# Performance work log

Hardware: AMD Instinct MI355X
Metric: run time of the kernel (lower is better)

Reference implementation:

```python
import jax, jax.numpy as jnp
import numpy as np
import math

B, S, D_IN, D_ATTN, D_HID = 4, 2048, 1024, 1024, 1024

def gelu_erf(x):
    return 0.5 * x * (1.0 + jax.lax.erf(x / math.sqrt(2.0)))

def setup_inputs() -> dict:
    key = jax.random.key(0)
    k = jax.random.split(key, 8)
    inputs = jax.random.normal(k[0], (B, S, D_IN), dtype=jnp.float32)
    attn_mask = jax.random.randint(k[1], (B, S, S), 0, 2, dtype=jnp.int32)
    sq = 1.0 / math.sqrt(D_IN)
    Wq = jax.random.normal(k[2], (D_IN, D_ATTN), dtype=jnp.float32) * sq
    bq = jnp.zeros((D_ATTN,), dtype=jnp.float32)
    Wk = jax.random.normal(k[3], (D_IN, D_ATTN), dtype=jnp.float32) * sq
    bk = jnp.zeros((D_ATTN,), dtype=jnp.float32)
    Wv = jax.random.normal(k[4], (D_IN, D_HID), dtype=jnp.float32) * sq
    bv = jnp.zeros((D_HID,), dtype=jnp.float32)
    return {"inputs": inputs, "attn_mask": attn_mask,
            "Wq": Wq, "bq": bq, "Wk": Wk, "bk": bk, "Wv": Wv, "bv": bv}

def reference(inputs, attn_mask, Wq, bq, Wk, bk, Wv, bv):
    # Q, K: [B, S, d_k]
    Q = inputs @ Wq + bq
    K = inputs @ Wk + bk
    scores = jnp.einsum('bqd,bkd->bqk', Q, K) / math.sqrt(D_ATTN)
    scores = scores + attn_mask.astype(scores.dtype) * (-1e9)
    attn = jax.nn.softmax(scores, axis=-1)
    WV = gelu_erf(inputs @ Wv + bv)           # [B, S, hidden]
    context = jnp.einsum('bqk,bkh->bqh', attn, WV)
    return (context, attn)
```

## Files before the change

kernel.cpp:

```cpp
#include <hip/hip_runtime.h>
#include <hip/hip_bf16.h>
#include <math.h>

#define B_   4
#define S_   2048
#define DIN  1024
#define DATT 1024
#define DHID 1024

typedef short bf16x8 __attribute__((ext_vector_type(8)));
typedef float f32x4  __attribute__((ext_vector_type(4)));

__device__ inline unsigned short f2bf(float f) {
    unsigned u = __float_as_uint(f);
    u += 0x7fffu + ((u >> 16) & 1u);
    return (unsigned short)(u >> 16);
}
__device__ inline float bf2f(unsigned u16) {
    return __uint_as_float(u16 << 16);
}
__device__ inline void gld16(const void* g, void* l) {
    __builtin_amdgcn_global_load_lds(
        (const __attribute__((address_space(1))) unsigned int*)g,
        (__attribute__((address_space(3))) unsigned int*)l, 16, 0, 0);
}

__device__ inline void xmap(int& bx, int& by, int& z)
{
    int gx = gridDim.x, gy = gridDim.y;
    int nwg = gx * gy * gridDim.z;
    int lin = blockIdx.x + gx * (blockIdx.y + gy * blockIdx.z);
    int s = (nwg & 7) ? lin : ((lin & 7) * (nwg >> 3) + (lin >> 3));
    if (!(gx & 3) && !(gy & 1)) {
        int cpz = (gx >> 2) * (gy >> 1);
        int chunk = s >> 3, w = s & 7;
        int cz = chunk / cpz, c2 = chunk % cpz;
        int cx = c2 % (gx >> 2), cy = c2 / (gx >> 2);
        bx = cx * 4 + (w & 3);
        by = cy * 2 + (w >> 2);
        z  = cz;
    } else {
        bx = s % gx;
        int t = s / gx;
        by = t % gy;
        z  = t / gy;
    }
}

__global__ __launch_bounds__(256)
void prep_k(const float* __restrict__ x, unsigned short* __restrict__ xb,
            const float* __restrict__ Wq, const float* __restrict__ Wk,
            const float* __restrict__ Wv, unsigned short* __restrict__ Wt,
            const int* __restrict__ m, unsigned* __restrict__ mb)
{
    const int b = blockIdx.x;
    const int tid = threadIdx.x;
    if (b < 4096) {
        int i = b * 256 + tid;
        const float4* p = (const float4*)x + (size_t)i * 2;
        float4 v0 = p[0], v1 = p[1];
        uint4 o;
        o.x = (unsigned)f2bf(v0.x) | ((unsigned)f2bf(v0.y) << 16);
        o.y = (unsigned)f2bf(v0.z) | ((unsigned)f2bf(v0.w) << 16);
        o.z = (unsigned)f2bf(v1.x) | ((unsigned)f2bf(v1.y) << 16);
        o.w = (unsigned)f2bf(v1.z) | ((unsigned)f2bf(v1.w) << 16);
        ((uint4*)xb)[i] = o;
    } else if (b < 4864) {
        int idx = b - 4096;
        int w = idx >> 8;
        const float* W = (w == 0) ? Wq : ((w == 1) ? Wk : Wv);
        unsigned short* D = Wt + (size_t)w * DIN * DATT;
        int t = (idx & 255) * 256 + tid;
        int n  = t >> 6;
        int kc = (t & 63) * 16;
        unsigned short r[16];
#pragma unroll
        for (int i = 0; i < 16; ++i) r[i] = f2bf(W[(size_t)(kc + i) * DATT + n]);
        uint4 o0, o1;
        o0.x = (unsigned)r[0] | ((unsigned)r[1] << 16);  o0.y = (unsigned)r[2] | ((unsigned)r[3] << 16);
        o0.z = (unsigned)r[4] | ((unsigned)r[5] << 16);  o0.w = (unsigned)r[6] | ((unsigned)r[7] << 16);
        o1.x = (unsigned)r[8] | ((unsigned)r[9] << 16);  o1.y = (unsigned)r[10] | ((unsigned)r[11] << 16);
        o1.z = (unsigned)r[12] | ((unsigned)r[13] << 16); o1.w = (unsigned)r[14] | ((unsigned)r[15] << 16);
        *(uint4*)(D + (size_t)n * DIN + kc)     = o0;
        *(uint4*)(D + (size_t)n * DIN + kc + 8) = o1;
    } else {
        int w = (b - 4864) * 256 + tid;
        const uint4* p = (const uint4*)(m + (size_t)w * 32);
        unsigned bits = 0;
#pragma unroll
        for (int g = 0; g < 8; ++g) {
            uint4 v = p[g];
            bits |= (v.x ? 1u : 0u) << (g * 4 + 0);
            bits |= (v.y ? 1u : 0u) << (g * 4 + 1);
            bits |= (v.z ? 1u : 0u) << (g * 4 + 2);
            bits |= (v.w ? 1u : 0u) << (g * 4 + 3);
        }
        mb[w] = bits;
    }
}

template<int EPI>
__global__ __launch_bounds__(512, 4)
void gemmS_k(const unsigned short* __restrict__ Ap, const unsigned short* __restrict__ Bp,
             const float* __restrict__ b0, const float* __restrict__ b1,
             const float* __restrict__ b2, const unsigned* __restrict__ mbits,
             void* __restrict__ Cp, void* __restrict__ Cp2,
             int K, int lda, int ldb, int ldc,
             long aStride, long bStride, long cStride, float scale)
{
    __shared__ __align__(16) unsigned short Al[256][64];
    __shared__ __align__(16) unsigned short Bl[128][64];

    int bx, by, z;
    xmap(bx, by, z);
    const int tid  = threadIdx.x;
    const int row0 = by * 256;
    const int col0 = bx * 128;
    const int wid  = tid >> 6, lane = tid & 63;
    const int lr = lane & 15, lg = lane >> 4;
    const int wm = wid >> 1, wn = wid & 1;
    const int wb = (tid & 448) * 16;

    const unsigned short* Ab = Ap + (size_t)aStride * z;
    const unsigned short* Bb = Bp + (size_t)bStride * z;

    f32x4 acc[4][4] = {};
    const int nt = K >> 6;

    const int srow = tid >> 3, sj = tid & 7;

    for (int t = 0; t < nt; ++t) {
        const int k0 = t << 6;
#pragma unroll
        for (int r = 0; r < 4; ++r) {
            int row = r * 64 + srow;
            gld16(Ab + (size_t)(row0 + row) * lda + k0 + ((sj ^ (row & 7)) << 3),
                  (char*)&Al[0][0] + r * 8192 + wb);
        }
#pragma unroll
        for (int r = 0; r < 2; ++r) {
            int row = r * 64 + srow;
            gld16(Bb + (size_t)(col0 + row) * ldb + k0 + ((sj ^ (row & 7)) << 3),
                  (char*)&Bl[0][0] + r * 8192 + wb);
        }
        __syncthreads();
#pragma unroll
        for (int s = 0; s < 2; ++s) {
            bf16x8 av[4], bv[4];
#pragma unroll
            for (int i = 0; i < 4; ++i) {
                int ra = wm * 64 + i * 16 + lr;
                av[i] = *(const bf16x8*)((const char*)&Al[0][0] + ra * 128 + ((((s << 2) | lg) ^ (ra & 7)) << 4));
                int rb = wn * 64 + i * 16 + lr;
                bv[i] = *(const bf16x8*)((const char*)&Bl[0][0] + rb * 128 + ((((s << 2) | lg) ^ (rb & 7)) << 4));
            }
#pragma unroll
            for (int mi = 0; mi < 4; ++mi)
#pragma unroll
                for (int ni = 0; ni < 4; ++ni)
                    acc[mi][ni] = __builtin_amdgcn_mfma_f32_16x16x32_bf16(av[mi], bv[ni], acc[mi][ni], 0, 0, 0);
        }
        __syncthreads();
    }

    unsigned short* scr = &Al[0][0] + wid * 2048;

    if (EPI == 6) {
        int w = col0 >> 10;
        if (w < 2) {
            unsigned short* C = (unsigned short*)Cp + (size_t)w * ((size_t)B_ * S_ * DATT);
            const float* bias = w ? b1 : b0;
            int cb0 = (col0 & 1023) + wn * 64;
#pragma unroll
            for (int h = 0; h < 2; ++h) {
#pragma unroll
                for (int mm = 0; mm < 2; ++mm) {
                    int mi = h * 2 + mm;
#pragma unroll
                    for (int ni = 0; ni < 4; ++ni) {
                        int lcol = ni * 16 + lr;
                        float bb = bias[cb0 + lcol];
#pragma unroll
                        for (int v = 0; v < 4; ++v) {
                            int wrow = mm * 16 + lg * 4 + v;
                            scr[wrow * 64 + (((lcol >> 3) ^ (wrow & 7)) << 3) + (lcol & 7)] =
                                f2bf(acc[mi][ni][v] + bb);
                        }
                    }
                }
                asm volatile("s_waitcnt lgkmcnt(0)" ::: "memory");
#pragma unroll
                for (int rr = 0; rr < 4; ++rr) {
                    int lrow = rr * 8 + (lane >> 3);
                    int chunk = lane & 7;
                    uint4 u = *(const uint4*)&scr[lrow * 64 + ((chunk ^ (lrow & 7)) << 3)];
                    int grow = row0 + wm * 64 + h * 32 + lrow;
                    *(uint4*)(C + (size_t)grow * DATT + cb0 + chunk * 8) = u;
                }
                asm volatile("s_waitcnt lgkmcnt(0)" ::: "memory");
            }
        } else {
            unsigned short* C = (unsigned short*)Cp2;
            int zz = row0 >> 11;
            int sb0 = (row0 & 2047) + wm * 64;
            int hb0 = (col0 & 1023) + wn * 64;
#pragma unroll
            for (int h = 0; h < 2; ++h) {
#pragma unroll
                for (int nn = 0; nn < 2; ++nn) {
                    int ni = h * 2 + nn;
                    int lcol = nn * 16 + lr;
                    float bb = b2[hb0 + h * 32 + lcol];
#pragma unroll
                    for (int mi = 0; mi < 4; ++mi)
#pragma unroll
                        for (int v = 0; v < 4; ++v) {
                            int lrow = mi * 16 + lg * 4 + v;
                            float xv = acc[mi][ni][v] + bb;
                            xv = 0.5f * xv * (1.0f + erff(xv * 0.70710678118654752f));
                            scr[lcol * 64 + (((lrow >> 3) ^ (lcol & 7)) << 3) + (lrow & 7)] = f2bf(xv);
                        }
                }
                asm volatile("s_waitcnt lgkmcnt(0)" ::: "memory");
#pragma unroll
                for (int rr = 0; rr < 4; ++rr) {
                    int lhid = rr * 8 + (lane >> 3);
                    int chunk = lane & 7;
                    uint4 u = *(const uint4*)&scr[lhid * 64 + ((chunk ^ (lhid & 7)) << 3)];
                    int ghid = hb0 + h * 32 + lhid;
                    *(uint4*)(C + ((size_t)zz * DHID + ghid) * S_ + sb0 + chunk * 8) = u;
                }
                asm volatile("s_waitcnt lgkmcnt(0)" ::: "memory");
            }
        }
    } else {
        unsigned short* C = (unsigned short*)Cp + (size_t)cStride * z;
        const unsigned* mb = mbits + (size_t)z * (S_ * S_ / 32);
        const int wbase = (col0 + wn * 64) >> 5;
#pragma unroll
        for (int h = 0; h < 2; ++h) {
#pragma unroll
            for (int mm = 0; mm < 2; ++mm) {
                int mi = h * 2 + mm;
#pragma unroll
                for (int v = 0; v < 4; ++v) {
                    int row = row0 + wm * 64 + mi * 16 + lg * 4 + v;
                    unsigned w0 = mb[(size_t)row * (S_ / 32) + wbase];
                    unsigned w1 = mb[(size_t)row * (S_ / 32) + wbase + 1];
                    int wrow = mm * 16 + lg * 4 + v;
#pragma unroll
                    for (int ni = 0; ni < 4; ++ni) {
                        int lcol = ni * 16 + lr;
                        unsigned wsel = (ni & 2) ? w1 : w0;
                        float ev = ((wsel >> ((ni & 1) * 16 + lr)) & 1)
                                 ? 0.0f : __expf(acc[mi][ni][v] * scale);
                        scr[wrow * 64 + (((lcol >> 3) ^ (wrow & 7)) << 3) + (lcol & 7)] = f2bf(ev);
                    }
                }
            }
            asm volatile("s_waitcnt lgkmcnt(0)" ::: "memory");
#pragma unroll
            for (int rr = 0; rr < 4; ++rr) {
                int lrow = rr * 8 + (lane >> 3);
                int chunk = lane & 7;
                uint4 u = *(const uint4*)&scr[lrow * 64 + ((chunk ^ (lrow & 7)) << 3)];
                int grow = row0 + wm * 64 + h * 32 + lrow;
                *(uint4*)(C + (size_t)grow * ldc + col0 + wn * 64 + chunk * 8) = u;
            }
            asm volatile("s_waitcnt lgkmcnt(0)" ::: "memory");
        }
    }
}

template<int AMODE, int EPI>
__global__ __launch_bounds__(256)
void gemm_k(const void* __restrict__ Ap, const unsigned short* __restrict__ Bp,
            const float* __restrict__ b0, const float* __restrict__ b1,
            const float* __restrict__ b2, const int* __restrict__ maskp,
            void* __restrict__ Cp, void* __restrict__ Cp2,
            int K, int lda, int ldb, int ldc,
            long aStride, long bStride, long cStride, long mStride, float scale)
{
    __shared__ __align__(16) unsigned short sh[2][2][128][64];
    int bx, by, z;
    xmap(bx, by, z);
    const int tid  = threadIdx.x;
    const int row0 = by * 128;
    const int col0 = bx * 128;
    const int wave = tid >> 6, lane = tid & 63;
    const int lr = lane & 15, lg = lane >> 4;
    const int wm = (wave >> 1) * 64, wn = (wave & 1) * 64;
    const unsigned short* Bb = Bp + (size_t)bStride * z;
    f32x4 acc[4][4] = {};
    const int nt = K >> 6;
    auto stage = [&](int b, int k0) {
        if (AMODE == 0) {
            const unsigned short* A = (const unsigned short*)Ap + (size_t)aStride * z;
#pragma unroll
            for (int q = 0; q < 4; ++q) {
                int c = q * 256 + tid;
                int row = c >> 3, j = c & 7;
                gld16((const char*)(A + (size_t)(row0 + row) * lda + k0) + ((j ^ (row & 7)) << 4),
                      (char*)&sh[b][0][0][0] + ((q * 256 + (tid & 192)) << 4));
            }
        } else {
            const float* A = (const float*)Ap + (size_t)aStride * z;
#pragma unroll
            for (int q = 0; q < 4; ++q) {
                int c = q * 256 + tid;
                int row = c >> 3, j = c & 7;
                const float* src = A + (size_t)(row0 + row) * lda + k0 + ((j ^ (row & 7)) << 3);
                float4 v0 = *(const float4*)src;
                float4 v1 = *(const float4*)(src + 4);
                uint4 p;
                p.x = (unsigned)f2bf(v0.x) | ((unsigned)f2bf(v0.y) << 16);
                p.y = (unsigned)f2bf(v0.z) | ((unsigned)f2bf(v0.w) << 16);
                p.z = (unsigned)f2bf(v1.x) | ((unsigned)f2bf(v1.y) << 16);
                p.w = (unsigned)f2bf(v1.z) | ((unsigned)f2bf(v1.w) << 16);
                *(uint4*)((char*)&sh[b][0][0][0] + ((size_t)c << 4)) = p;
            }
        }
#pragma unroll
        for (int q = 0; q < 4; ++q) {
            int c = q * 256 + tid;
            int row = c >> 3, j = c & 7;
            gld16((const char*)(Bb + (size_t)(col0 + row) * ldb + k0) + ((j ^ (row & 7)) << 4),
                  (char*)&sh[b][1][0][0] + ((q * 256 + (tid & 192)) << 4));
        }
    };
    stage(0, 0);
    __syncthreads();
    int cur = 0;
    for (int t = 0; t < nt; ++t) {
        if (t + 1 < nt) stage(cur ^ 1, (t + 1) << 6);
        const char* baseA = (const char*)&sh[cur][0][0][0];
        const char* baseB = (const char*)&sh[cur][1][0][0];
        bf16x8 af[2][4], bfv[2][4];
#pragma unroll
        for (int s = 0; s < 2; ++s)
#pragma unroll
            for (int i = 0; i < 4; ++i) {
                int ra = wm + i * 16 + lr;
                af[s][i]  = *(const bf16x8*)(baseA + ra * 128 + ((((s << 2) | lg) ^ (ra & 7)) << 4));
                int rb = wn + i * 16 + lr;
                bfv[s][i] = *(const bf16x8*)(baseB + rb * 128 + ((((s << 2) | lg) ^ (rb & 7)) << 4));
            }
#pragma unroll
        for (int s = 0; s < 2; ++s)
#pragma unroll
            for (int mi = 0; mi < 4; ++mi)
#pragma unroll
                for (int ni = 0; ni < 4; ++ni)
                    acc[mi][ni] = __builtin_amdgcn_mfma_f32_16x16x32_bf16(af[s][mi], bfv[s][ni], acc[mi][ni], 0, 0, 0);
        if (t + 1 < nt) __syncthreads();
        cur ^= 1;
    }
    if (EPI == 6) {
        int w = col0 >> 10;
        int cb = (col0 & 1023) + wn;
        if (w < 2) {
            unsigned short* C = (unsigned short*)Cp + (size_t)w * ((size_t)B_ * S_ * DATT);
            const float* bias = w ? b1 : b0;
#pragma unroll
            for (int mi = 0; mi < 4; ++mi)
#pragma unroll
                for (int ni = 0; ni < 4; ++ni) {
                    int col = cb + ni * 16 + lr;
                    float bb = bias[col];
                    int rowb = row0 + wm + mi * 16 + lg * 4;
#pragma unroll
                    for (int v = 0; v < 4; ++v)
                        C[(size_t)(rowb + v) * DATT + col] = f2bf(acc[mi][ni][v] + bb);
                }
        } else {
            unsigned short* C = (unsigned short*)Cp2;
            int zz = row0 >> 11;
            int sb = (row0 & 2047) + wm;
#pragma unroll
            for (int mi = 0; mi < 4; ++mi)
#pragma unroll
                for (int ni = 0; ni < 4; ++ni) {
                    int col = cb + ni * 16 + lr;
                    float bb = b2[col];
                    unsigned short r[4];
#pragma unroll
                    for (int v = 0; v < 4; ++v) {
                        float xv = acc[mi][ni][v] + bb;
                        xv = 0.5f * xv * (1.0f + erff(xv * 0.70710678118654752f));
                        r[v] = f2bf(xv);
                    }
                    uint2 o;
                    o.x = (unsigned)r[0] | ((unsigned)r[1] << 16);
                    o.y = (unsigned)r[2] | ((unsigned)r[3] << 16);
                    *(uint2*)(C + ((size_t)zz * DHID + col) * S_ + sb + mi * 16 + lg * 4) = o;
                }
        }
    } else if (EPI == 5) {
        float* C = (float*)Cp + (size_t)cStride * z;
        const float* invs = b0 + (size_t)z * S_;
#pragma unroll
        for (int mi = 0; mi < 4; ++mi)
#pragma unroll
            for (int ni = 0; ni < 4; ++ni) {
                int col = col0 + wn + ni * 16 + lr;
                int rowb = row0 + wm + mi * 16 + lg * 4;
#pragma unroll
                for (int v = 0; v < 4; ++v)
                    C[(size_t)(rowb + v) * ldc + col] = acc[mi][ni][v] * invs[rowb + v];
            }
    } else {
        float* C = (float*)Cp + (size_t)cStride * z;
        const int* mp = (EPI == 2) ? (maskp + (size_t)mStride * z) : nullptr;
#pragma unroll
        for (int mi = 0; mi < 4; ++mi)
#pragma unroll
            for (int ni = 0; ni < 4; ++ni) {
                int col = col0 + wn + ni * 16 + lr;
                int rowb = row0 + wm + mi * 16 + lg * 4;
#pragma unroll
                for (int v = 0; v < 4; ++v) {
                    float val = acc[mi][ni][v];
                    if (EPI == 2) val = val * scale + (float)mp[(size_t)(rowb + v) * ldc + col] * (-1e9f);
                    C[(size_t)(rowb + v) * ldc + col] = val;
                }
            }
    }
}

__global__ __launch_bounds__(256)
void rownormM_k(const unsigned short* __restrict__ e, float* __restrict__ attn,
                float* __restrict__ invs)
{
    const int row = blockIdx.x;
    const int tid = threadIdx.x;
    uint4 u = ((const uint4*)(e + (size_t)row * S_))[tid];
    float f[8];
    f[0] = bf2f(u.x & 0xffffu); f[1] = bf2f(u.x >> 16);
    f[2] = bf2f(u.y & 0xffffu); f[3] = bf2f(u.y >> 16);
    f[4] = bf2f(u.z & 0xffffu); f[5] = bf2f(u.z >> 16);
    f[6] = bf2f(u.w & 0xffffu); f[7] = bf2f(u.w >> 16);
    float s = ((f[0] + f[1]) + (f[2] + f[3])) + ((f[4] + f[5]) + (f[6] + f[7]));
#pragma unroll
    for (int o = 32; o; o >>= 1) s += __shfl_xor(s, o);
    __shared__ float red[4];
    if ((tid & 63) == 0) red[tid >> 6] = s;
    __syncthreads();
    s = (red[0] + red[1]) + (red[2] + red[3]);
    float inv = 1.0f / s;
    float* p = attn + (size_t)row * S_;
    ((float4*)p)[tid * 2]     = make_float4(f[0] * inv, f[1] * inv, f[2] * inv, f[3] * inv);
    ((float4*)p)[tid * 2 + 1] = make_float4(f[4] * inv, f[5] * inv, f[6] * inv, f[7] * inv);
    if (tid == 0) invs[row] = inv;
}

template<bool WRITEATTN>
__global__ __launch_bounds__(256)
void rownorm_k(const unsigned short* __restrict__ e, float* __restrict__ attn,
               float* __restrict__ invs)
{
    const int row = blockIdx.x;
    const int tid = threadIdx.x;
    uint4 u = ((const uint4*)(e + (size_t)row * S_))[tid];
    float f[8];
    f[0] = bf2f(u.x & 0xffffu); f[1] = bf2f(u.x >> 16);
    f[2] = bf2f(u.y & 0xffffu); f[3] = bf2f(u.y >> 16);
    f[4] = bf2f(u.z & 0xffffu); f[5] = bf2f(u.z >> 16);
    f[6] = bf2f(u.w & 0xffffu); f[7] = bf2f(u.w >> 16);
    float s = ((f[0] + f[1]) + (f[2] + f[3])) + ((f[4] + f[5]) + (f[6] + f[7]));
#pragma unroll
    for (int o = 32; o; o >>= 1) s += __shfl_xor(s, o);
    __shared__ float red[4];
    if ((tid & 63) == 0) red[tid >> 6] = s;
    __syncthreads();
    s = (red[0] + red[1]) + (red[2] + red[3]);
    float inv = 1.0f / s;
    if (WRITEATTN) {
        float* p = attn + (size_t)row * S_;
        ((float4*)p)[tid * 2]     = make_float4(f[0] * inv, f[1] * inv, f[2] * inv, f[3] * inv);
        ((float4*)p)[tid * 2 + 1] = make_float4(f[4] * inv, f[5] * inv, f[6] * inv, f[7] * inv);
    } else {
        if (tid == 0) invs[row] = inv;
    }
}

__global__ __launch_bounds__(256)
void softmax_k(float* __restrict__ attn)
{
    const int row = blockIdx.x;
    float* p = attn + (size_t)row * S_;
    const int tid = threadIdx.x;
    float4 a = ((const float4*)p)[tid * 2];
    float4 b = ((const float4*)p)[tid * 2 + 1];
    float m = fmaxf(fmaxf(fmaxf(a.x, a.y), fmaxf(a.z, a.w)),
                    fmaxf(fmaxf(b.x, b.y), fmaxf(b.z, b.w)));
#pragma unroll
    for (int o = 32; o; o >>= 1) m = fmaxf(m, __shfl_xor(m, o));
    __shared__ float redm[4];
    __shared__ float reds[4];
    if ((tid & 63) == 0) redm[tid >> 6] = m;
    __syncthreads();
    m = fmaxf(fmaxf(redm[0], redm[1]), fmaxf(redm[2], redm[3]));
    float e[8];
    e[0] = expf(a.x - m); e[1] = expf(a.y - m); e[2] = expf(a.z - m); e[3] = expf(a.w - m);
    e[4] = expf(b.x - m); e[5] = expf(b.y - m); e[6] = expf(b.z - m); e[7] = expf(b.w - m);
    float s = e[0] + e[1] + e[2] + e[3] + e[4] + e[5] + e[6] + e[7];
#pragma unroll
    for (int o = 32; o; o >>= 1) s += __shfl_xor(s, o);
    if ((tid & 63) == 0) reds[tid >> 6] = s;
    __syncthreads();
    s = reds[0] + reds[1] + reds[2] + reds[3];
    float inv = 1.0f / s;
    ((float4*)p)[tid * 2]     = make_float4(e[0] * inv, e[1] * inv, e[2] * inv, e[3] * inv);
    ((float4*)p)[tid * 2 + 1] = make_float4(e[4] * inv, e[5] * inv, e[6] * inv, e[7] * inv);
}

extern "C" void kernel_launch(void* const* d_in, const int* in_sizes, int n_in,
                              void* d_out, int out_size, void* d_ws, size_t ws_size,
                              hipStream_t stream)
{
    const float* x    = (const float*)d_in[0];
    const int*   mask = (const int*)d_in[1];
    const float* Wq   = (const float*)d_in[2];
    const float* bq   = (const float*)d_in[3];
    const float* Wk   = (const float*)d_in[4];
    const float* bk   = (const float*)d_in[5];
    const float* Wv   = (const float*)d_in[6];
    const float* bv   = (const float*)d_in[7];

    float* ctx  = (float*)d_out;
    float* attn = ctx + (size_t)B_ * S_ * DHID;

    unsigned short* Qb = (unsigned short*)ctx;
    unsigned short* Kb = Qb + (size_t)B_ * S_ * DATT;
    unsigned short* Xb = (unsigned short*)attn;
    unsigned short* Wb = Xb + (size_t)B_ * S_ * DIN;

    const size_t eElems  = (size_t)B_ * S_ * S_;
    const size_t mWords  = eElems / 32;
    const size_t wvElems = (size_t)B_ * DHID * S_;

    size_t needFast = eElems * 2 + (size_t)B_ * S_ * 4 + mWords * 4 + wvElems * 2 + 256;
    size_t needMid  = eElems * 2 + (size_t)B_ * S_ * 4 + mWords * 4 + 256;

    dim3 blk(256), blk5(512);

    if (ws_size >= needFast) {
        unsigned short* e    = (unsigned short*)d_ws;
        float*          invs = (float*)(e + eElems);
        unsigned*       mb   = (unsigned*)(invs + (size_t)B_ * S_);
        unsigned short* WVbT = (unsigned short*)(mb + mWords);

        prep_k<<<dim3(6912), blk, 0, stream>>>(x, Xb, Wq, Wk, Wv, Wb, mask, mb);
        gemmS_k<6><<<dim3(24, 32, 1), blk5, 0, stream>>>(
            Xb, Wb, bq, bk, bv, nullptr, Qb, WVbT,
            DIN, DIN, DIN, 0, 0, 0, 0, 1.0f);
        gemmS_k<4><<<dim3(16, 8, 4), blk5, 0, stream>>>(
            Qb, Kb, nullptr, nullptr, nullptr, mb, e, nullptr,
            DATT, DATT, DATT, S_,
            (long)S_ * DATT, (long)S_ * DATT, (long)S_ * S_, 0.03125f);
        rownormM_k<<<dim3(B_ * S_), blk, 0, stream>>>(e, attn, invs);
        gemm_k<0, 5><<<dim3(8, 16, 4), blk, 0, stream>>>(
            e, WVbT, invs, nullptr, nullptr, nullptr, ctx, nullptr,
            S_, S_, S_, DHID,
            (long)S_ * S_, (long)DHID * S_, (long)S_ * DHID, 0, 1.0f);
    } else if (ws_size >= needMid) {
        unsigned short* e    = (unsigned short*)d_ws;
        float*          invs = (float*)(e + eElems);
        unsigned*       mb   = (unsigned*)(invs + (size_t)B_ * S_);
        unsigned short* WVbT = Wb + (size_t)3 * DIN * DATT;

        prep_k<<<dim3(6912), blk, 0, stream>>>(x, Xb, Wq, Wk, Wv, Wb, mask, mb);
        gemmS_k<6><<<dim3(24, 32, 1), blk5, 0, stream>>>(
            Xb, Wb, bq, bk, bv, nullptr, Qb, WVbT,
            DIN, DIN, DIN, 0, 0, 0, 0, 1.0f);
        gemmS_k<4><<<dim3(16, 8, 4), blk5, 0, stream>>>(
            Qb, Kb, nullptr, nullptr, nullptr, mb, e, nullptr,
            DATT, DATT, DATT, S_,
            (long)S_ * DATT, (long)S_ * DATT, (long)S_ * S_, 0.03125f);
        rownorm_k<false><<<dim3(B_ * S_), blk, 0, stream>>>(e, nullptr, invs);
        gemm_k<0, 5><<<dim3(8, 16, 4), blk, 0, stream>>>(
            e, WVbT, invs, nullptr, nullptr, nullptr, ctx, nullptr,
            S_, S_, S_, DHID,
            (long)S_ * S_, (long)DHID * S_, (long)S_ * DHID, 0, 1.0f);
        rownorm_k<true><<<dim3(B_ * S_), blk, 0, stream>>>(e, attn, nullptr);
    } else {
        unsigned short* WVw = (unsigned short*)d_ws;
        prep_k<<<dim3(4864), blk, 0, stream>>>(x, Xb, Wq, Wk, Wv, Wb, mask, nullptr);
        gemm_k<0, 6><<<dim3(24, 64, 1), blk, 0, stream>>>(
            Xb, Wb, bq, bk, bv, nullptr, Qb, WVw,
            DIN, DIN, DIN, 0, 0, 0, 0, 0, 1.0f);
        gemm_k<0, 2><<<dim3(16, 16, 4), blk, 0, stream>>>(
            Qb, Kb, nullptr, nullptr, nullptr, mask, attn, nullptr,
            DATT, DATT, DATT, S_,
            (long)S_ * DATT, (long)S_ * DATT, (long)S_ * S_, (long)S_ * S_, 0.03125f);
        softmax_k<<<dim3(B_ * S_), blk, 0, stream>>>(attn);
        gemm_k<1, 3><<<dim3(8, 16, 4), blk, 0, stream>>>(
            attn, WVw, nullptr, nullptr, nullptr, nullptr, ctx, nullptr,
            S_, S_, S_, DHID,
            (long)S_ * S_, (long)DHID * S_, (long)S_ * DHID, 0, 1.0f);
    }
}
```

Before: 210.9 us.

## Fuse softmax row sums into score GEMM and attn write into context GEMM

The score GEMM epilogue now accumulates per-row sums of the masked exponentials with shuffles and atomics, so the separate row-normalisation pass over the bf16 exp matrix is removed. A tiny kernel inverts the sums. The context GEMM moves to the larger 256x128 gemmS tile. While it streams the exp tiles through LDS, the blocks whose column index matches write the normalised fp32 attn output, so e is read only once. The costs are atomic contention, a memset, and extra global stores inside the GEMM main loop. The atomic float additions also make the row sums order-dependent.

```diff
diff --git a/kernel.cpp b/kernel.cpp
--- a/kernel.cpp
+++ b/kernel.cpp
@@ -99,6 +99,13 @@
     }
 }
 
+__global__ __launch_bounds__(256)
+void invert_k(float* __restrict__ p)
+{
+    int i = blockIdx.x * 256 + threadIdx.x;
+    p[i] = 1.0f / p[i];
+}
+
 template<int EPI>
 __global__ __launch_bounds__(512, 4)
 void gemmS_k(const unsigned short* __restrict__ Ap, const unsigned short* __restrict__ Bp,
@@ -160,6 +167,30 @@
                 for (int ni = 0; ni < 4; ++ni)
                     acc[mi][ni] = __builtin_amdgcn_mfma_f32_16x16x32_bf16(av[mi], bv[ni], acc[mi][ni], 0, 0, 0);
         }
+        if (EPI == 7 && (t >> 2) == bx) {
+            int tt = t & 3;
+            int r = tid >> 1, half = tid & 1;
+            float inv = b0[(size_t)z * S_ + row0 + r];
+            float* aout = (float*)Cp2 + ((size_t)z * S_ + row0 + r) * S_
+                        + (size_t)bx * 256 + tt * 64 + half * 32;
+            const unsigned short* arow = &Al[r][0];
+#pragma unroll
+            for (int g = 0; g < 4; ++g) {
+                int grp = half * 4 + g;
+                bf16x8 vv = *(const bf16x8*)(arow + ((grp ^ (r & 7)) << 3));
+                float4 lo, hi;
+                lo.x = bf2f((unsigned short)vv[0]) * inv;
+                lo.y = bf2f((unsigned short)vv[1]) * inv;
+                lo.z = bf2f((unsigned short)vv[2]) * inv;
+                lo.w = bf2f((unsigned short)vv[3]) * inv;
+                hi.x = bf2f((unsigned short)vv[4]) * inv;
+                hi.y = bf2f((unsigned short)vv[5]) * inv;
+                hi.z = bf2f((unsigned short)vv[6]) * inv;
+                hi.w = bf2f((unsigned short)vv[7]) * inv;
+                *(float4*)(aout + g * 8)     = lo;
+                *(float4*)(aout + g * 8 + 4) = hi;
+            }
+        }
         __syncthreads();
     }
 
@@ -233,8 +264,9 @@
                 asm volatile("s_waitcnt lgkmcnt(0)" ::: "memory");
             }
         }
-    } else {
+    } else if (EPI == 4) {
         unsigned short* C = (unsigned short*)Cp + (size_t)cStride * z;
+        float* rs = (float*)Cp2 + (size_t)z * S_;
         const unsigned* mb = mbits + (size_t)z * (S_ * S_ / 32);
         const int wbase = (col0 + wn * 64) >> 5;
 #pragma unroll
@@ -248,14 +280,22 @@
                     unsigned w0 = mb[(size_t)row * (S_ / 32) + wbase];
                     unsigned w1 = mb[(size_t)row * (S_ / 32) + wbase + 1];
                     int wrow = mm * 16 + lg * 4 + v;
+                    float evs[4];
 #pragma unroll
                     for (int ni = 0; ni < 4; ++ni) {
                         int lcol = ni * 16 + lr;
                         unsigned wsel = (ni & 2) ? w1 : w0;
                         float ev = ((wsel >> ((ni & 1) * 16 + lr)) & 1)
                                  ? 0.0f : __expf(acc[mi][ni][v] * scale);
+                        evs[ni] = ev;
                         scr[wrow * 64 + (((lcol >> 3) ^ (wrow & 7)) << 3) + (lcol & 7)] = f2bf(ev);
                     }
+                    float s4 = (evs[0] + evs[1]) + (evs[2] + evs[3]);
+                    s4 += __shfl_xor(s4, 1);
+                    s4 += __shfl_xor(s4, 2);
+                    s4 += __shfl_xor(s4, 4);
+                    s4 += __shfl_xor(s4, 8);
+                    if (lr == 0) atomicAdd(rs + row, s4);
                 }
             }
             asm volatile("s_waitcnt lgkmcnt(0)" ::: "memory");
@@ -268,6 +308,22 @@
                 *(uint4*)(C + (size_t)grow * ldc + col0 + wn * 64 + chunk * 8) = u;
             }
             asm volatile("s_waitcnt lgkmcnt(0)" ::: "memory");
+        }
+    } else {
+        float* C = (float*)Cp + (size_t)cStride * z;
+        const float* invp = b0 + (size_t)z * S_;
+#pragma unroll
+        for (int mi = 0; mi < 4; ++mi) {
+            int rowb = row0 + wm * 64 + mi * 16 + lg * 4;
+#pragma unroll
+            for (int v = 0; v < 4; ++v) {
+                float inv = invp[rowb + v];
+#pragma unroll
+                for (int ni = 0; ni < 4; ++ni) {
+                    int col = col0 + wn * 64 + ni * 16 + lr;
+                    C[(size_t)(rowb + v) * ldc + col] = acc[mi][ni][v] * inv;
+                }
+            }
         }
     }
 }
@@ -427,32 +483,6 @@
     }
 }
 
-__global__ __launch_bounds__(256)
-void rownormM_k(const unsigned short* __restrict__ e, float* __restrict__ attn,
-                float* __restrict__ invs)
-{
-    const int row = blockIdx.x;
-    const int tid = threadIdx.x;
-    uint4 u = ((const uint4*)(e + (size_t)row * S_))[tid];
-    float f[8];
-    f[0] = bf2f(u.x & 0xffffu); f[1] = bf2f(u.x >> 16);
-    f[2] = bf2f(u.y & 0xffffu); f[3] = bf2f(u.y >> 16);
-    f[4] = bf2f(u.z & 0xffffu); f[5] = bf2f(u.z >> 16);
-    f[6] = bf2f(u.w & 0xffffu); f[7] = bf2f(u.w >> 16);
-    float s = ((f[0] + f[1]) + (f[2] + f[3])) + ((f[4] + f[5]) + (f[6] + f[7]));
-#pragma unroll
-    for (int o = 32; o; o >>= 1) s += __shfl_xor(s, o);
-    __shared__ float red[4];
-    if ((tid & 63) == 0) red[tid >> 6] = s;
-    __syncthreads();
-    s = (red[0] + red[1]) + (red[2] + red[3]);
-    float inv = 1.0f / s;
-    float* p = attn + (size_t)row * S_;
-    ((float4*)p)[tid * 2]     = make_float4(f[0] * inv, f[1] * inv, f[2] * inv, f[3] * inv);
-    ((float4*)p)[tid * 2 + 1] = make_float4(f[4] * inv, f[5] * inv, f[6] * inv, f[7] * inv);
-    if (tid == 0) invs[row] = inv;
-}
-
 template<bool WRITEATTN>
 __global__ __launch_bounds__(256)
 void rownorm_k(const unsigned short* __restrict__ e, float* __restrict__ attn,
@@ -551,18 +581,19 @@
         unsigned short* WVbT = (unsigned short*)(mb + mWords);
 
         prep_k<<<dim3(6912), blk, 0, stream>>>(x, Xb, Wq, Wk, Wv, Wb, mask, mb);
+        hipMemsetAsync(invs, 0, (size_t)B_ * S_ * 4, stream);
         gemmS_k<6><<<dim3(24, 32, 1), blk5, 0, stream>>>(
             Xb, Wb, bq, bk, bv, nullptr, Qb, WVbT,
             DIN, DIN, DIN, 0, 0, 0, 0, 1.0f);
         gemmS_k<4><<<dim3(16, 8, 4), blk5, 0, stream>>>(
-            Qb, Kb, nullptr, nullptr, nullptr, mb, e, nullptr,
+            Qb, Kb, nullptr, nullptr, nullptr, mb, e, invs,
             DATT, DATT, DATT, S_,
             (long)S_ * DATT, (long)S_ * DATT, (long)S_ * S_, 0.03125f);
-        rownormM_k<<<dim3(B_ * S_), blk, 0, stream>>>(e, attn, invs);
-        gemm_k<0, 5><<<dim3(8, 16, 4), blk, 0, stream>>>(
-            e, WVbT, invs, nullptr, nullptr, nullptr, ctx, nullptr,
+        invert_k<<<dim3(B_ * S_ / 256), blk, 0, stream>>>(invs);
+        gemmS_k<7><<<dim3(8, 8, 4), blk5, 0, stream>>>(
+            e, WVbT, invs, nullptr, nullptr, nullptr, ctx, attn,
             S_, S_, S_, DHID,
-            (long)S_ * S_, (long)DHID * S_, (long)S_ * DHID, 0, 1.0f);
+            (long)S_ * S_, (long)DHID * S_, (long)S_ * DHID, 1.0f);
     } else if (ws_size >= needMid) {
         unsigned short* e    = (unsigned short*)d_ws;
         float*          invs = (float*)(e + eElems);
@@ -570,14 +601,15 @@
         unsigned short* WVbT = Wb + (size_t)3 * DIN * DATT;
 
         prep_k<<<dim3(6912), blk, 0, stream>>>(x, Xb, Wq, Wk, Wv, Wb, mask, mb);
+        hipMemsetAsync(invs, 0, (size_t)B_ * S_ * 4, stream);
         gemmS_k<6><<<dim3(24, 32, 1), blk5, 0, stream>>>(
             Xb, Wb, bq, bk, bv, nullptr, Qb, WVbT,
             DIN, DIN, DIN, 0, 0, 0, 0, 1.0f);
         gemmS_k<4><<<dim3(16, 8, 4), blk5, 0, stream>>>(
-            Qb, Kb, nullptr, nullptr, nullptr, mb, e, nullptr,
+            Qb, Kb, nullptr, nullptr, nullptr, mb, e, invs,
             DATT, DATT, DATT, S_,
             (long)S_ * DATT, (long)S_ * DATT, (long)S_ * S_, 0.03125f);
-        rownorm_k<false><<<dim3(B_ * S_), blk, 0, stream>>>(e, nullptr, invs);
+        invert_k<<<dim3(B_ * S_ / 256), blk, 0, stream>>>(invs);
         gemm_k<0, 5><<<dim3(8, 16, 4), blk, 0, stream>>>(
             e, WVbT, invs, nullptr, nullptr, nullptr, ctx, nullptr,
             S_, S_, S_, DHID,
```

Result: slower. 224.4 us (+6.4%).

## Use 256-thread wide-accumulator kernel for masked QK^T exp scores

Applied to the files above, without the earlier changes.

Adds a dedicated QK^T GEMM kernel with 256 threads per block, in which each wave computes a 128x64 sub-tile (8x4 MFMA fragments), replacing the 512-thread gemmS_k<4> for the score stage on the fast path. The epilogue applies the bit-packed mask and exp, then stages bf16 results through LDS with a swizzle for coalesced 16-byte stores. Larger per-wave tiles raise MFMA work per LDS fragment load but use many more accumulator registers, which lowers occupancy and leaves a single-buffered K loop with fewer waves to hide latency.

```diff
diff --git a/kernel.cpp b/kernel.cpp
--- a/kernel.cpp
+++ b/kernel.cpp
@@ -99,6 +99,108 @@
     }
 }
 
+__global__ __launch_bounds__(256, 2)
+void gemmW_k(const unsigned short* __restrict__ Ap, const unsigned short* __restrict__ Bp,
+             const unsigned* __restrict__ mbits, unsigned short* __restrict__ Cp,
+             int K, int lda, int ldb, int ldc,
+             long aStride, long bStride, long cStride, float scale)
+{
+    __shared__ __align__(16) unsigned short Al[256][64];
+    __shared__ __align__(16) unsigned short Bl[128][64];
+
+    int bx, by, z;
+    xmap(bx, by, z);
+    const int tid  = threadIdx.x;
+    const int row0 = by * 256;
+    const int col0 = bx * 128;
+    const int wid  = tid >> 6, lane = tid & 63;
+    const int lr = lane & 15, lg = lane >> 4;
+    const int wm = wid >> 1, wn = wid & 1;
+    const int wb = (tid & 192) * 16;
+
+    const unsigned short* Ab = Ap + (size_t)aStride * z;
+    const unsigned short* Bb = Bp + (size_t)bStride * z;
+
+    f32x4 acc[8][4] = {};
+    const int nt = K >> 6;
+
+    const int srow = tid >> 3, sj = tid & 7;
+
+    for (int t = 0; t < nt; ++t) {
+        const int k0 = t << 6;
+#pragma unroll
+        for (int r = 0; r < 8; ++r) {
+            int row = r * 32 + srow;
+            gld16(Ab + (size_t)(row0 + row) * lda + k0 + ((sj ^ (row & 7)) << 3),
+                  (char*)&Al[0][0] + r * 4096 + wb);
+        }
+#pragma unroll
+        for (int r = 0; r < 4; ++r) {
+            int row = r * 32 + srow;
+            gld16(Bb + (size_t)(col0 + row) * ldb + k0 + ((sj ^ (row & 7)) << 3),
+                  (char*)&Bl[0][0] + r * 4096 + wb);
+        }
+        __syncthreads();
+#pragma unroll
+        for (int s = 0; s < 2; ++s) {
+            bf16x8 av[8], bv[4];
+#pragma unroll
+            for (int i = 0; i < 8; ++i) {
+                int ra = wm * 128 + i * 16 + lr;
+                av[i] = *(const bf16x8*)((const char*)&Al[0][0] + ra * 128 + ((((s << 2) | lg) ^ (ra & 7)) << 4));
+            }
+#pragma unroll
+            for (int i = 0; i < 4; ++i) {
+                int rb = wn * 64 + i * 16 + lr;
+                bv[i] = *(const bf16x8*)((const char*)&Bl[0][0] + rb * 128 + ((((s << 2) | lg) ^ (rb & 7)) << 4));
+            }
+#pragma unroll
+            for (int mi = 0; mi < 8; ++mi)
+#pragma unroll
+                for (int ni = 0; ni < 4; ++ni)
+                    acc[mi][ni] = __builtin_amdgcn_mfma_f32_16x16x32_bf16(av[mi], bv[ni], acc[mi][ni], 0, 0, 0);
+        }
+        __syncthreads();
+    }
+
+    unsigned short* scr = &Al[0][0] + wid * 2048;
+    unsigned short* C = Cp + (size_t)cStride * z;
+    const unsigned* mb = mbits + (size_t)z * (S_ * S_ / 32);
+    const int wbase = (col0 + wn * 64) >> 5;
+#pragma unroll
+    for (int h = 0; h < 4; ++h) {
+#pragma unroll
+        for (int mm = 0; mm < 2; ++mm) {
+            int mi = h * 2 + mm;
+#pragma unroll
+            for (int v = 0; v < 4; ++v) {
+                int row = row0 + wm * 128 + mi * 16 + lg * 4 + v;
+                unsigned w0 = mb[(size_t)row * (S_ / 32) + wbase];
+                unsigned w1 = mb[(size_t)row * (S_ / 32) + wbase + 1];
+                int wrow = mm * 16 + lg * 4 + v;
+#pragma unroll
+                for (int ni = 0; ni < 4; ++ni) {
+                    int lcol = ni * 16 + lr;
+                    unsigned wsel = (ni & 2) ? w1 : w0;
+                    float ev = ((wsel >> ((ni & 1) * 16 + lr)) & 1)
+                             ? 0.0f : __expf(acc[mi][ni][v] * scale);
+                    scr[wrow * 64 + (((lcol >> 3) ^ (wrow & 7)) << 3) + (lcol & 7)] = f2bf(ev);
+                }
+            }
+        }
+        asm volatile("s_waitcnt lgkmcnt(0)" ::: "memory");
+#pragma unroll
+        for (int rr = 0; rr < 4; ++rr) {
+            int lrow = rr * 8 + (lane >> 3);
+            int chunk = lane & 7;
+            uint4 u = *(const uint4*)&scr[lrow * 64 + ((chunk ^ (lrow & 7)) << 3)];
+            int grow = row0 + wm * 128 + h * 32 + lrow;
+            *(uint4*)(C + (size_t)grow * ldc + col0 + wn * 64 + chunk * 8) = u;
+        }
+        asm volatile("s_waitcnt lgkmcnt(0)" ::: "memory");
+    }
+}
+
 template<int EPI>
 __global__ __launch_bounds__(512, 4)
 void gemmS_k(const unsigned short* __restrict__ Ap, const unsigned short* __restrict__ Bp,
@@ -554,8 +656,8 @@
         gemmS_k<6><<<dim3(24, 32, 1), blk5, 0, stream>>>(
             Xb, Wb, bq, bk, bv, nullptr, Qb, WVbT,
             DIN, DIN, DIN, 0, 0, 0, 0, 1.0f);
-        gemmS_k<4><<<dim3(16, 8, 4), blk5, 0, stream>>>(
-            Qb, Kb, nullptr, nullptr, nullptr, mb, e, nullptr,
+        gemmW_k<<<dim3(16, 8, 4), blk, 0, stream>>>(
+            Qb, Kb, mb, e,
             DATT, DATT, DATT, S_,
             (long)S_ * DATT, (long)S_ * DATT, (long)S_ * S_, 0.03125f);
         rownormM_k<<<dim3(B_ * S_), blk, 0, stream>>>(e, attn, invs);
```

Measured after the change: 212.2 us. Within noise of the previous version (+0.6%).
